# Kernel optimization log

Measured on AMD Instinct MI355X. Metric: run time of the kernel, lower is better.

## Reference

```python
import jax, jax.numpy as jnp
import numpy as np
from jax import lax

WIN = 7
PAD = WIN // 2
K1, K2 = 0.01, 0.03
NP = WIN * WIN
COV_NORM = NP / (NP - 1)  # use_sample_covariance=True


def _dwconv(x, w, channel):
    # depthwise 2D conv, SAME-style explicit padding (torch conv2d padding=pad)
    return lax.conv_general_dilated(
        x, w, window_strides=(1, 1),
        padding=[(PAD, PAD), (PAD, PAD)],
        feature_group_count=channel,
        dimension_numbers=('NCHW', 'OIHW', 'NCHW'))


def setup_inputs() -> dict:
    key = jax.random.key(0)
    k1, k2 = jax.random.split(key)
    B, C, H, W = 64, 1, 384, 384
    gt = jax.random.uniform(k1, (B, C, H, W), dtype=jnp.float32)
    pred = jax.random.uniform(k2, (B, C, H, W), dtype=jnp.float32)
    # uniform (box) window: create_window(7, channel=1, gaussian_weights=False)
    window = jnp.ones((C, 1, WIN, WIN), dtype=jnp.float32) / NP
    return {"gt": gt, "pred": pred, "window": window}


def reference(gt, pred, window):
    channel = gt.shape[1]
    data_range = jnp.max(gt)  # data_range=None default

    ux = _dwconv(gt, window, channel)
    uy = _dwconv(pred, window, channel)
    uxx = _dwconv(gt * gt, window, channel) - ux * ux
    uyy = _dwconv(pred * pred, window, channel) - uy * uy
    uxy = _dwconv(gt * pred, window, channel) - ux * uy

    vx = COV_NORM * uxx
    vy = COV_NORM * uyy
    vxy = COV_NORM * uxy

    C1 = (K1 * data_range) ** 2
    C2 = (K2 * data_range) ** 2

    S = (2.0 * ux * uy + C1) * (2.0 * vxy + C2) / ((ux * ux + uy * uy + C1) * (vx + vy + C2))
    ssim_map = S[:, :, PAD:-PAD, PAD:-PAD]
    return jnp.mean(ssim_map)  # size_average=True, full=False
```

## Files before the change

### kernel.cpp

```cpp
#include <hip/hip_runtime.h>


#define PADW 3
#define BT 64
#define BAND 22
#define NCHUNK 4

constexpr int B_ = 64, H_ = 384, W_ = 384;
constexpr int W2 = W_ / 2;
constexpr int OUTD = W_ - 2 * PADW;
constexpr int NBANDS = (OUTD + BAND - 1) / BAND;
constexpr int NTILES = 3;
constexpr int TOTAL_BLOCKS = NTILES * NBANDS * B_;
constexpr double NPIX = (double)B_ * OUTD * OUTD;

__device__ __forceinline__ unsigned enc_f(float f) {
    unsigned u = __float_as_uint(f);
    return (u & 0x80000000u) ? ~u : (u | 0x80000000u);
}
__device__ __forceinline__ float dec_f(unsigned e) {
    return __uint_as_float((e & 0x80000000u) ? (e & 0x7fffffffu) : ~e);
}

__device__ __forceinline__ float2 f2add(float2 a, float2 b) { return make_float2(a.x + b.x, a.y + b.y); }
__device__ __forceinline__ float2 f2sub(float2 a, float2 b) { return make_float2(a.x - b.x, a.y - b.y); }

__device__ __forceinline__ void glds16(const void* g, void* l) {
    __builtin_amdgcn_global_load_lds(
        (const __attribute__((address_space(1))) void*)g,
        (__attribute__((address_space(3))) void*)l, 16, 0, 0);
}

__global__ void __launch_bounds__(256)
max_kernel(const float4* __restrict__ g4, unsigned* ws_max, int n4) {
    int tid = blockIdx.x * blockDim.x + threadIdx.x;
    int stride = gridDim.x * blockDim.x;
    float m = -3.402823466e38f;
    for (int i = tid; i < n4; i += stride) {
        float4 v = g4[i];
        m = fmaxf(m, fmaxf(fmaxf(v.x, v.y), fmaxf(v.z, v.w)));
    }
#pragma unroll
    for (int off = 32; off > 0; off >>= 1)
        m = fmaxf(m, __shfl_down(m, off));
    __shared__ float sm[4];
    if ((threadIdx.x & 63) == 0) sm[threadIdx.x >> 6] = m;
    __syncthreads();
    if (threadIdx.x == 0) {
        float mm = fmaxf(fmaxf(sm[0], sm[1]), fmaxf(sm[2], sm[3]));
        atomicMax(ws_max, enc_f(mm));
    }
}

__device__ __forceinline__ float ssim_px(float sx, float sy, float sxx, float syy, float sxy,
                                         float C1, float C2) {
    const float inv49 = 1.0f / 49.0f;
    const float covn  = 49.0f / 48.0f;
    float ux  = sx * inv49, uy = sy * inv49;
    float uxx = sxx * inv49 - ux * ux;
    float uyy = syy * inv49 - uy * uy;
    float uxy = sxy * inv49 - ux * uy;
    float vvx = covn * uxx, vvy = covn * uyy, vvxy = covn * uxy;
    float num = (2.0f * ux * uy + C1) * (2.0f * vvxy + C2);
    float den = (ux * ux + uy * uy + C1) * (vvx + vvy + C2);
    return num / den;
}

__global__ void __launch_bounds__(BT)
ssim_kernel(const float* __restrict__ gt, const float* __restrict__ pred,
            const unsigned* __restrict__ ws_max, double* __restrict__ ws_part) {
    const int t    = threadIdx.x;
    const int tile = blockIdx.x;
    const int band = blockIdx.y;
    const int b    = blockIdx.z;
    const int bid  = (b * NBANDS + band) * NTILES + tile;

    const float dr = dec_f(*ws_max);
    const float C1 = (0.01f * dr) * (0.01f * dr);
    const float C2 = (0.03f * dr) * (0.03f * dr);

    const int  row0   = band * BAND;
    const int  cbase2 = tile * 63;
    const int  base2  = cbase2 & ~1;
    const int  off    = cbase2 & 1;
    const int  maxoff = W_ * 4 - base2 * 8 - 16;
    const bool active = (t < 63);

    __shared__ __align__(16) float2 sgA[7][68], spA[7][68];
    __shared__ __align__(16) float2 sgB[7][68], spB[7][68];

    float2 rx[7], ry[7], rxx[7], ryy[7], rxy[7];
#pragma unroll
    for (int j = 0; j < 7; ++j) {
        rx[j] = make_float2(0.f, 0.f); ry[j] = rx[j];
        rxx[j] = rx[j]; ryy[j] = rx[j]; rxy[j] = rx[j];
    }
    float2 vx = make_float2(0.f, 0.f), vy = vx, vxx = vx, vyy = vx, vxy = vx;
    double acc = 0.0;

    const float2* gbase = (const float2*)(gt   + (size_t)b * H_ * W_);
    const float2* pbase = (const float2*)(pred + (size_t)b * H_ * W_);

    const int laneoff = min(t * 16, maxoff);

    auto stage = [&](float2 (*dg)[68], float2 (*dp)[68], int c) {
        const int r0 = row0 + c * 7;
#pragma unroll
        for (int j = 0; j < 7; ++j) {
            const int ir = min(r0 + j, H_ - 1);
            const char* grb = (const char*)(gbase + (size_t)ir * W2 + base2);
            const char* prb = (const char*)(pbase + (size_t)ir * W2 + base2);
            if (t < 34) {
                glds16(grb + laneoff, &dg[j][0]);
                glds16(prb + laneoff, &dp[j][0]);
            }
        }
    };

    auto compute = [&](const float2 (*sg)[68], const float2 (*sp)[68], int c) {
#pragma unroll
        for (int j = 0; j < 7; ++j) {
            const int ti = t + off;
            float2 d0 = sg[j][ti], d1 = sg[j][ti + 1], d2 = sg[j][ti + 2], d3 = sg[j][ti + 3];
            float2 e0 = sp[j][ti], e1 = sp[j][ti + 1], e2 = sp[j][ti + 2], e3 = sp[j][ti + 3];

            float hx0 = d0.x + d0.y + d1.x + d1.y + d2.x + d2.y + d3.x;
            float hy0 = e0.x + e0.y + e1.x + e1.y + e2.x + e2.y + e3.x;
            float hxx0 = fmaf(d0.x, d0.x, fmaf(d0.y, d0.y, fmaf(d1.x, d1.x,
                         fmaf(d1.y, d1.y, fmaf(d2.x, d2.x, fmaf(d2.y, d2.y, d3.x * d3.x))))));
            float hyy0 = fmaf(e0.x, e0.x, fmaf(e0.y, e0.y, fmaf(e1.x, e1.x,
                         fmaf(e1.y, e1.y, fmaf(e2.x, e2.x, fmaf(e2.y, e2.y, e3.x * e3.x))))));
            float hxy0 = fmaf(d0.x, e0.x, fmaf(d0.y, e0.y, fmaf(d1.x, e1.x,
                         fmaf(d1.y, e1.y, fmaf(d2.x, e2.x, fmaf(d2.y, e2.y, d3.x * e3.x))))));

            float2 h_x  = make_float2(hx0,  hx0  - d0.x        + d3.y);
            float2 h_y  = make_float2(hy0,  hy0  - e0.x        + e3.y);
            float2 h_xx = make_float2(hxx0, hxx0 - d0.x * d0.x + d3.y * d3.y);
            float2 h_yy = make_float2(hyy0, hyy0 - e0.x * e0.x + e3.y * e3.y);
            float2 h_xy = make_float2(hxy0, hxy0 - d0.x * e0.x + d3.y * e3.y);

            vx  = f2add(vx,  f2sub(h_x,  rx[j]));  rx[j]  = h_x;
            vy  = f2add(vy,  f2sub(h_y,  ry[j]));  ry[j]  = h_y;
            vxx = f2add(vxx, f2sub(h_xx, rxx[j])); rxx[j] = h_xx;
            vyy = f2add(vyy, f2sub(h_yy, ryy[j])); ryy[j] = h_yy;
            vxy = f2add(vxy, f2sub(h_xy, rxy[j])); rxy[j] = h_xy;

            const int i = c * 7 + j;
            if (i >= 6) {
                const int orow = row0 + i - 6;
                if (active && orow < OUTD) {
                    acc += (double)ssim_px(vx.x, vy.x, vxx.x, vyy.x, vxy.x, C1, C2)
                         + (double)ssim_px(vx.y, vy.y, vxx.y, vyy.y, vxy.y, C1, C2);
                }
            }
        }
    };

    stage(sgA, spA, 0);
    stage(sgB, spB, 1);
    compute(sgA, spA, 0);
    stage(sgA, spA, 2);
    compute(sgB, spB, 1);
    stage(sgB, spB, 3);
    compute(sgA, spA, 2);
    compute(sgB, spB, 3);

#pragma unroll
    for (int off2 = 32; off2 > 0; off2 >>= 1)
        acc += __shfl_down(acc, off2);
    if (t == 0) ws_part[bid] = acc;
}

__global__ void __launch_bounds__(256)
final_kernel(const double* __restrict__ ws_part, float* __restrict__ out) {
    const int t = threadIdx.x;
    double s = 0.0;
    for (int i = t; i < TOTAL_BLOCKS; i += 256) s += ws_part[i];
#pragma unroll
    for (int off = 32; off > 0; off >>= 1)
        s += __shfl_down(s, off);
    __shared__ double sd[4];
    if ((t & 63) == 0) sd[t >> 6] = s;
    __syncthreads();
    if (t == 0) out[0] = (float)((sd[0] + sd[1] + sd[2] + sd[3]) / NPIX);
}

extern "C" void kernel_launch(void* const* d_in, const int* in_sizes, int n_in,
                              void* d_out, int out_size, void* d_ws, size_t ws_size,
                              hipStream_t stream) {
    const float* gt   = (const float*)d_in[0];
    const float* pred = (const float*)d_in[1];
    float* out = (float*)d_out;

    unsigned* ws_max  = (unsigned*)d_ws;
    double*   ws_part = (double*)((char*)d_ws + 64);


    const int n4 = B_ * H_ * W_ / 4;
    max_kernel<<<1024, 256, 0, stream>>>((const float4*)gt, ws_max, n4);

    dim3 grid(NTILES, NBANDS, B_);
    ssim_kernel<<<grid, BT, 0, stream>>>(gt, pred, ws_max, ws_part);

    final_kernel<<<1, 256, 0, stream>>>(ws_part, out);
}
```

Baseline: 136.8 us.

## Fuse max reduction into SSIM kernel via cooperative grid sync and taller bands

Removes the separate max kernel launch: each block issues its first LDS tile loads, takes part in a grid-stride max over gt, then waits on a cooperative grid barrier before reading the data range. A non-cooperative fallback keeps the old two-kernel path if the cooperative launch fails. Band height grows from 22 to 40 rows, with the chunk loop rolled, to cut the vertical halo re-read overhead. The trade-offs are fewer blocks of 64 threads and therefore lower occupancy, plus the cost of a grid-wide barrier and the requirement that every block be co-resident.

```diff
diff --git a/kernel.cpp b/kernel.cpp
--- a/kernel.cpp
+++ b/kernel.cpp
@@ -1,10 +1,13 @@
 #include <hip/hip_runtime.h>
+#include <hip/hip_cooperative_groups.h>
+
+namespace cg = cooperative_groups;
 
 
 #define PADW 3
 #define BT 64
-#define BAND 22
-#define NCHUNK 4
+#define BAND 40
+#define NCHUNK 7
 
 constexpr int B_ = 64, H_ = 384, W_ = 384;
 constexpr int W2 = W_ / 2;
@@ -12,6 +15,7 @@
 constexpr int NBANDS = (OUTD + BAND - 1) / BAND;
 constexpr int NTILES = 3;
 constexpr int TOTAL_BLOCKS = NTILES * NBANDS * B_;
+constexpr int N4 = B_ * H_ * W_ / 4;
 constexpr double NPIX = (double)B_ * OUTD * OUTD;
 
 __device__ __forceinline__ unsigned enc_f(float f) {
@@ -67,17 +71,13 @@
 }
 
 __global__ void __launch_bounds__(BT)
-ssim_kernel(const float* __restrict__ gt, const float* __restrict__ pred,
-            const unsigned* __restrict__ ws_max, double* __restrict__ ws_part) {
+fused_kernel(const float* __restrict__ gt, const float* __restrict__ pred,
+             unsigned* __restrict__ ws_max, double* __restrict__ ws_part, int coop) {
     const int t    = threadIdx.x;
     const int tile = blockIdx.x;
     const int band = blockIdx.y;
     const int b    = blockIdx.z;
     const int bid  = (b * NBANDS + band) * NTILES + tile;
-
-    const float dr = dec_f(*ws_max);
-    const float C1 = (0.01f * dr) * (0.01f * dr);
-    const float C2 = (0.03f * dr) * (0.03f * dr);
 
     const int  row0   = band * BAND;
     const int  cbase2 = tile * 63;
@@ -97,6 +97,7 @@
     }
     float2 vx = make_float2(0.f, 0.f), vy = vx, vxx = vx, vyy = vx, vxy = vx;
     double acc = 0.0;
+    float C1 = 0.f, C2 = 0.f;
 
     const float2* gbase = (const float2*)(gt   + (size_t)b * H_ * W_);
     const float2* pbase = (const float2*)(pred + (size_t)b * H_ * W_);
@@ -146,24 +147,45 @@
             vxy = f2add(vxy, f2sub(h_xy, rxy[j])); rxy[j] = h_xy;
 
             const int i = c * 7 + j;
-            if (i >= 6) {
-                const int orow = row0 + i - 6;
-                if (active && orow < OUTD) {
-                    acc += (double)ssim_px(vx.x, vy.x, vxx.x, vyy.x, vxy.x, C1, C2)
-                         + (double)ssim_px(vx.y, vy.y, vxx.y, vyy.y, vxy.y, C1, C2);
-                }
+            const int orow = row0 + i - 6;
+            if (i >= 6 && (i - 6) < BAND && active && orow < OUTD) {
+                acc += (double)ssim_px(vx.x, vy.x, vxx.x, vyy.x, vxy.x, C1, C2)
+                     + (double)ssim_px(vx.y, vy.y, vxx.y, vyy.y, vxy.y, C1, C2);
             }
         }
     };
 
     stage(sgA, spA, 0);
     stage(sgB, spB, 1);
-    compute(sgA, spA, 0);
-    stage(sgA, spA, 2);
-    compute(sgB, spB, 1);
-    stage(sgB, spB, 3);
-    compute(sgA, spA, 2);
-    compute(sgB, spB, 3);
+
+    if (coop) {
+        const float4* g4 = (const float4*)gt;
+        float m = -3.402823466e38f;
+        for (int i = bid * BT + t; i < N4; i += TOTAL_BLOCKS * BT) {
+            float4 v = g4[i];
+            m = fmaxf(m, fmaxf(fmaxf(v.x, v.y), fmaxf(v.z, v.w)));
+        }
+#pragma unroll
+        for (int o = 32; o > 0; o >>= 1)
+            m = fmaxf(m, __shfl_down(m, o));
+        if (t == 0) atomicMax(ws_max, enc_f(m));
+        cg::this_grid().sync();
+    }
+
+    {
+        const float dr = dec_f(__hip_atomic_load(ws_max, __ATOMIC_RELAXED,
+                                                 __HIP_MEMORY_SCOPE_AGENT));
+        C1 = (0.01f * dr) * (0.01f * dr);
+        C2 = (0.03f * dr) * (0.03f * dr);
+    }
+
+#pragma unroll 1
+    for (int c = 0; c < NCHUNK; c += 2) {
+        compute(sgA, spA, c);
+        if (c + 2 < NCHUNK) stage(sgA, spA, c + 2);
+        if (c + 1 < NCHUNK) compute(sgB, spB, c + 1);
+        if (c + 3 < NCHUNK) stage(sgB, spB, c + 3);
+    }
 
 #pragma unroll
     for (int off2 = 32; off2 > 0; off2 >>= 1)
@@ -196,11 +218,16 @@
     double*   ws_part = (double*)((char*)d_ws + 64);
 
 
-    const int n4 = B_ * H_ * W_ / 4;
-    max_kernel<<<1024, 256, 0, stream>>>((const float4*)gt, ws_max, n4);
-
     dim3 grid(NTILES, NBANDS, B_);
-    ssim_kernel<<<grid, BT, 0, stream>>>(gt, pred, ws_max, ws_part);
+    int coop = 1;
+    void* args[] = {(void*)&gt, (void*)&pred, (void*)&ws_max, (void*)&ws_part, (void*)&coop};
+    hipError_t e = hipLaunchCooperativeKernel((void*)fused_kernel, grid, dim3(BT),
+                                              args, 0, stream);
+    if (e != hipSuccess) {
+        (void)hipGetLastError();
+        max_kernel<<<1024, 256, 0, stream>>>((const float4*)gt, ws_max, N4);
+        fused_kernel<<<grid, BT, 0, stream>>>(gt, pred, ws_max, ws_part, 0);
+    }
 
     final_kernel<<<1, 256, 0, stream>>>(ws_part, out);
 }
```

After: 329.1 us. 141% more time.

## Load whole band halo into LDS upfront and shrink row band

Applied to the files above, without the earlier changes.

Replaces the two-buffer staged load/compute schedule with one upfront async global-to-LDS load of all band rows plus halo. The band height drops from 22 to 15 output rows so that 21 staged rows fit one buffer. The max-value read is moved after the loads are issued so its latency overlaps them. The aim is more blocks in flight and a simpler load schedule, at the cost of a larger halo re-read fraction and no overlap between loading and compute inside a block.

```diff
diff --git a/kernel.cpp b/kernel.cpp
--- a/kernel.cpp
+++ b/kernel.cpp
@@ -3,8 +3,8 @@
 
 #define PADW 3
 #define BT 64
-#define BAND 22
-#define NCHUNK 4
+#define BAND 15
+#define SROWS (BAND + 6)
 
 constexpr int B_ = 64, H_ = 384, W_ = 384;
 constexpr int W2 = W_ / 2;
@@ -75,10 +75,6 @@
     const int b    = blockIdx.z;
     const int bid  = (b * NBANDS + band) * NTILES + tile;
 
-    const float dr = dec_f(*ws_max);
-    const float C1 = (0.01f * dr) * (0.01f * dr);
-    const float C2 = (0.03f * dr) * (0.03f * dr);
-
     const int  row0   = band * BAND;
     const int  cbase2 = tile * 63;
     const int  base2  = cbase2 & ~1;
@@ -86,8 +82,27 @@
     const int  maxoff = W_ * 4 - base2 * 8 - 16;
     const bool active = (t < 63);
 
-    __shared__ __align__(16) float2 sgA[7][68], spA[7][68];
-    __shared__ __align__(16) float2 sgB[7][68], spB[7][68];
+    __shared__ __align__(16) float2 sg[SROWS][68], sp[SROWS][68];
+
+    const float2* gbase = (const float2*)(gt   + (size_t)b * H_ * W_);
+    const float2* pbase = (const float2*)(pred + (size_t)b * H_ * W_);
+
+    const int laneoff = min(t * 16, maxoff);
+
+    if (t < 34) {
+#pragma unroll
+        for (int r = 0; r < SROWS; ++r) {
+            const int ir = min(row0 + r, H_ - 1);
+            const char* grb = (const char*)(gbase + (size_t)ir * W2 + base2);
+            const char* prb = (const char*)(pbase + (size_t)ir * W2 + base2);
+            glds16(grb + laneoff, &sg[r][0]);
+            glds16(prb + laneoff, &sp[r][0]);
+        }
+    }
+
+    const float dr = dec_f(*ws_max);
+    const float C1 = (0.01f * dr) * (0.01f * dr);
+    const float C2 = (0.03f * dr) * (0.03f * dr);
 
     float2 rx[7], ry[7], rxx[7], ryy[7], rxy[7];
 #pragma unroll
@@ -98,31 +113,16 @@
     float2 vx = make_float2(0.f, 0.f), vy = vx, vxx = vx, vyy = vx, vxy = vx;
     double acc = 0.0;
 
-    const float2* gbase = (const float2*)(gt   + (size_t)b * H_ * W_);
-    const float2* pbase = (const float2*)(pred + (size_t)b * H_ * W_);
-
-    const int laneoff = min(t * 16, maxoff);
-
-    auto stage = [&](float2 (*dg)[68], float2 (*dp)[68], int c) {
-        const int r0 = row0 + c * 7;
+#pragma unroll 1
+    for (int g = 0; g < 3; ++g) {
 #pragma unroll
         for (int j = 0; j < 7; ++j) {
-            const int ir = min(r0 + j, H_ - 1);
-            const char* grb = (const char*)(gbase + (size_t)ir * W2 + base2);
-            const char* prb = (const char*)(pbase + (size_t)ir * W2 + base2);
-            if (t < 34) {
-                glds16(grb + laneoff, &dg[j][0]);
-                glds16(prb + laneoff, &dp[j][0]);
-            }
-        }
-    };
-
-    auto compute = [&](const float2 (*sg)[68], const float2 (*sp)[68], int c) {
-#pragma unroll
-        for (int j = 0; j < 7; ++j) {
+            const int i  = g * 7 + j;
             const int ti = t + off;
-            float2 d0 = sg[j][ti], d1 = sg[j][ti + 1], d2 = sg[j][ti + 2], d3 = sg[j][ti + 3];
-            float2 e0 = sp[j][ti], e1 = sp[j][ti + 1], e2 = sp[j][ti + 2], e3 = sp[j][ti + 3];
+            const float2* rg = sg[i];
+            const float2* rp = sp[i];
+            float2 d0 = rg[ti], d1 = rg[ti + 1], d2 = rg[ti + 2], d3 = rg[ti + 3];
+            float2 e0 = rp[ti], e1 = rp[ti + 1], e2 = rp[ti + 2], e3 = rp[ti + 3];
 
             float hx0 = d0.x + d0.y + d1.x + d1.y + d2.x + d2.y + d3.x;
             float hy0 = e0.x + e0.y + e1.x + e1.y + e2.x + e2.y + e3.x;
@@ -145,25 +145,13 @@
             vyy = f2add(vyy, f2sub(h_yy, ryy[j])); ryy[j] = h_yy;
             vxy = f2add(vxy, f2sub(h_xy, rxy[j])); rxy[j] = h_xy;
 
-            const int i = c * 7 + j;
-            if (i >= 6) {
-                const int orow = row0 + i - 6;
-                if (active && orow < OUTD) {
-                    acc += (double)ssim_px(vx.x, vy.x, vxx.x, vyy.x, vxy.x, C1, C2)
-                         + (double)ssim_px(vx.y, vy.y, vxx.y, vyy.y, vxy.y, C1, C2);
-                }
+            const int orow = row0 + i - 6;
+            if (i >= 6 && active && orow < OUTD) {
+                acc += (double)ssim_px(vx.x, vy.x, vxx.x, vyy.x, vxy.x, C1, C2)
+                     + (double)ssim_px(vx.y, vy.y, vxx.y, vyy.y, vxy.y, C1, C2);
             }
         }
-    };
-
-    stage(sgA, spA, 0);
-    stage(sgB, spB, 1);
-    compute(sgA, spA, 0);
-    stage(sgA, spA, 2);
-    compute(sgB, spB, 1);
-    stage(sgB, spB, 3);
-    compute(sgA, spA, 2);
-    compute(sgB, spB, 3);
+    }
 
 #pragma unroll
     for (int off2 = 32; off2 > 0; off2 >>= 1)
```

Result: slower. 145.1 us (+6.1%).
